# Kernel optimization log

Hardware: AMD Instinct MI355X
Metric: run time of the kernel (lower is better)

Reference implementation:

```python
import jax, jax.numpy as jnp
import numpy as np

CUTOFF = 5.0
P = 6               # envelope polynomial power
NUM_RBF = 6
NUM_SBF = 7
EMBED = 128
TYPE_EMBED = 64
OUT_EMBED = 256
INT_EMBED = 64      # angle_int_embed_size
BASIS_EMBED = 8
N_BLOCKS = 4
N_DENSE_OUT = 3
N_RES_BEFORE = 1
N_RES_AFTER = 2
N_SPECIES = 16
NUM_TARGETS = 1
N_ATOMS = 4096
N_EDGES = 65536
N_TRIPLETS = 524288

# first 6 positive roots of spherical Bessel j_l, l = 0..6
BESSEL_ZEROS = np.array([
    [3.141593, 6.283185, 9.424778, 12.566371, 15.707963, 18.849556],
    [4.493409, 7.725252, 10.904122, 14.066194, 17.220755, 20.371303],
    [5.763459, 9.095011, 12.322941, 15.514603, 18.689036, 21.853874],
    [6.987932, 10.417119, 13.698023, 16.923621, 20.121806, 23.304247],
    [8.182561, 11.704907, 15.039665, 18.301256, 21.525418, 24.727566],
    [9.355812, 12.966530, 16.354710, 19.653152, 22.904551, 26.126750],
    [10.512835, 14.207392, 17.647975, 20.983463, 24.262768, 27.507868]], dtype=np.float32)

act = jax.nn.silu  # swish


def envelope(x):
    a = -(P + 1) * (P + 2) / 2.0
    b = float(P * (P + 2))
    c = -P * (P + 1) / 2.0
    env = 1.0 / x + a * x ** (P - 1) + b * x ** P + c * x ** (P + 1)
    return jnp.where(x < 1.0, env, 0.0)


def radial_bessel(d):
    # d: (E,) -> (E, NUM_RBF)
    x = d / CUTOFF
    n = jnp.arange(1, NUM_RBF + 1, dtype=jnp.float32)
    return np.float32(np.sqrt(2.0 / CUTOFF)) * envelope(x)[:, None] * jnp.sin(jnp.pi * n[None, :] * x[:, None])


def spherical_basis(d_kj, angles, triplet_mask):
    # d_kj: (T,), angles: (T,) -> (T, NUM_SBF * NUM_RBF)
    x = jnp.maximum(d_kj / CUTOFF, 1e-6)
    env = envelope(x)
    zeros = jnp.asarray(BESSEL_ZEROS)
    radial = []
    for l in range(NUM_SBF):
        a = zeros[l][None, :] * x[:, None]           # (T, NUM_RBF)
        j0 = jnp.sin(a) / a
        if l == 0:
            radial.append(j0)
            continue
        j1 = jnp.sin(a) / a ** 2 - jnp.cos(a) / a
        jm2, jm1 = j0, j1
        for ll in range(2, l + 1):
            jm2, jm1 = jm1, (2 * ll - 1) / a * jm1 - jm2
        radial.append(jm1)
    radial = jnp.stack(radial, axis=1)               # (T, NUM_SBF, NUM_RBF)
    ct = jnp.cos(angles)
    Pl = [jnp.ones_like(ct), ct]
    for l in range(2, NUM_SBF):
        Pl.append(((2 * l - 1) * ct * Pl[l - 1] - (l - 1) * Pl[l - 2]) / l)
    sph = jnp.stack([np.float32(np.sqrt((2 * l + 1) / (4.0 * np.pi))) * Pl[l] for l in range(NUM_SBF)], axis=1)  # (T, NUM_SBF)
    sbf = (env[:, None, None] * radial * sph[:, :, None]).reshape(-1, NUM_SBF * NUM_RBF)
    return jnp.where(triplet_mask[:, None], sbf, 0.0)


def _forward(distances, angles, species_embed, emb_rbf_w, emb_rbf_b, emb_dense_w, emb_dense_b,
             out_rbf_w, out_up_w, out_dense_w, out_dense_b, out_final_w,
             int_ji_w, int_ji_b, int_kj_w, int_kj_b, int_rbf1_w, int_rbf2_w, int_down_w,
             int_sbf1_w, int_sbf2_w, int_up_w, int_res1_w, int_res1_b, int_skip_w, int_skip_b,
             int_res2_w, int_res2_b,
             species, idx_i, idx_j, reduce_to_ji, expand_to_kj, edge_mask, triplet_mask):
    n_particles = species.shape[0]
    n_edges = distances.shape[0]
    d = jnp.where(edge_mask, distances, 2.0 * CUTOFF)       # masked edges -> env = 0
    rbf = radial_bessel(d)                                  # (E, 6)
    sbf = spherical_basis(d[expand_to_kj], angles, triplet_mask)  # (T, 42)

    # embedding block
    h = species_embed[species]                              # (N, 64)
    rbf_emb = rbf @ emb_rbf_w + emb_rbf_b                   # (E, 128)
    m = act(jnp.concatenate([h[idx_j], h[idx_i], rbf_emb], axis=-1) @ emb_dense_w + emb_dense_b)

    def output_block(i, msg):
        atom = jax.ops.segment_sum((rbf @ out_rbf_w[i]) * msg, idx_i, num_segments=n_particles)
        atom = atom @ out_up_w[i]
        for k in range(N_DENSE_OUT):
            atom = act(atom @ out_dense_w[i, k] + out_dense_b[i, k])
        return atom @ out_final_w[i]

    out = output_block(0, m)
    for i in range(N_BLOCKS):
        x_ji = act(m @ int_ji_w[i] + int_ji_b[i])
        x_kj = act(m @ int_kj_w[i] + int_kj_b[i])
        x_kj = x_kj * ((rbf @ int_rbf1_w[i]) @ int_rbf2_w[i])
        x_kj = act(x_kj @ int_down_w[i])                    # (E, 64)
        x_kj = x_kj[expand_to_kj] * ((sbf @ int_sbf1_w[i]) @ int_sbf2_w[i])  # (T, 64)
        x_kj = jax.ops.segment_sum(x_kj, reduce_to_ji, num_segments=n_edges)
        x_kj = act(x_kj @ int_up_w[i])
        hm = x_ji + x_kj
        for r in range(N_RES_BEFORE):
            hm = hm + act(act(hm @ int_res1_w[i, r, 0] + int_res1_b[i, r, 0]) @ int_res1_w[i, r, 1] + int_res1_b[i, r, 1])
        m = act(hm @ int_skip_w[i] + int_skip_b[i]) + m
        for r in range(N_RES_AFTER):
            m = m + act(act(m @ int_res2_w[i, r, 0] + int_res2_b[i, r, 0]) @ int_res2_w[i, r, 1] + int_res2_b[i, r, 1])
        out = out + output_block(i + 1, m)
    return out


def setup_inputs() -> dict:
    key = jax.random.key(0)
    ks = iter(jax.random.split(key, 40))
    def nrm(shape, fan_in):
        return jax.random.normal(next(ks), shape, dtype=jnp.float32) / np.float32(np.sqrt(fan_in))
    inp = {}
    inp['distances'] = 0.5 + 4.45 * jax.random.uniform(next(ks), (N_EDGES,), dtype=jnp.float32)
    inp['angles'] = jnp.pi * jax.random.uniform(next(ks), (N_TRIPLETS,), dtype=jnp.float32)
    inp['species_embed'] = jax.random.normal(next(ks), (N_SPECIES, TYPE_EMBED), dtype=jnp.float32)
    inp['emb_rbf_w'] = nrm((NUM_RBF, EMBED), NUM_RBF)
    inp['emb_rbf_b'] = jnp.zeros((EMBED,), jnp.float32)
    inp['emb_dense_w'] = nrm((2 * TYPE_EMBED + EMBED, EMBED), 2 * TYPE_EMBED + EMBED)
    inp['emb_dense_b'] = jnp.zeros((EMBED,), jnp.float32)
    nb1 = N_BLOCKS + 1
    inp['out_rbf_w'] = nrm((nb1, NUM_RBF, EMBED), NUM_RBF)
    inp['out_up_w'] = nrm((nb1, EMBED, OUT_EMBED), EMBED)
    inp['out_dense_w'] = nrm((nb1, N_DENSE_OUT, OUT_EMBED, OUT_EMBED), OUT_EMBED)
    inp['out_dense_b'] = jnp.zeros((nb1, N_DENSE_OUT, OUT_EMBED), jnp.float32)
    inp['out_final_w'] = nrm((nb1, OUT_EMBED, NUM_TARGETS), OUT_EMBED)
    inp['int_ji_w'] = nrm((N_BLOCKS, EMBED, EMBED), EMBED)
    inp['int_ji_b'] = jnp.zeros((N_BLOCKS, EMBED), jnp.float32)
    inp['int_kj_w'] = nrm((N_BLOCKS, EMBED, EMBED), EMBED)
    inp['int_kj_b'] = jnp.zeros((N_BLOCKS, EMBED), jnp.float32)
    inp['int_rbf1_w'] = nrm((N_BLOCKS, NUM_RBF, BASIS_EMBED), NUM_RBF)
    inp['int_rbf2_w'] = nrm((N_BLOCKS, BASIS_EMBED, EMBED), BASIS_EMBED)
    inp['int_down_w'] = nrm((N_BLOCKS, EMBED, INT_EMBED), EMBED)
    inp['int_sbf1_w'] = nrm((N_BLOCKS, NUM_SBF * NUM_RBF, BASIS_EMBED), NUM_SBF * NUM_RBF)
    inp['int_sbf2_w'] = nrm((N_BLOCKS, BASIS_EMBED, INT_EMBED), BASIS_EMBED)
    inp['int_up_w'] = nrm((N_BLOCKS, INT_EMBED, EMBED), INT_EMBED)
    inp['int_res1_w'] = nrm((N_BLOCKS, N_RES_BEFORE, 2, EMBED, EMBED), EMBED)
    inp['int_res1_b'] = jnp.zeros((N_BLOCKS, N_RES_BEFORE, 2, EMBED), jnp.float32)
    inp['int_skip_w'] = nrm((N_BLOCKS, EMBED, EMBED), EMBED)
    inp['int_skip_b'] = jnp.zeros((N_BLOCKS, EMBED), jnp.float32)
    inp['int_res2_w'] = nrm((N_BLOCKS, N_RES_AFTER, 2, EMBED, EMBED), EMBED)
    inp['int_res2_b'] = jnp.zeros((N_BLOCKS, N_RES_AFTER, 2, EMBED), jnp.float32)
    inp['species'] = jax.random.randint(next(ks), (N_ATOMS,), 0, N_SPECIES)
    inp['idx_i'] = jax.random.randint(next(ks), (N_EDGES,), 0, N_ATOMS)
    inp['idx_j'] = jax.random.randint(next(ks), (N_EDGES,), 0, N_ATOMS)
    inp['reduce_to_ji'] = jax.random.randint(next(ks), (N_TRIPLETS,), 0, N_EDGES)
    inp['expand_to_kj'] = jax.random.randint(next(ks), (N_TRIPLETS,), 0, N_EDGES)
    inp['edge_mask'] = jnp.ones((N_EDGES,), dtype=bool)
    inp['triplet_mask'] = jnp.ones((N_TRIPLETS,), dtype=bool)
    return inp


def reference(distances, angles, species_embed, emb_rbf_w, emb_rbf_b, emb_dense_w, emb_dense_b,
              out_rbf_w, out_up_w, out_dense_w, out_dense_b, out_final_w,
              int_ji_w, int_ji_b, int_kj_w, int_kj_b, int_rbf1_w, int_rbf2_w, int_down_w,
              int_sbf1_w, int_sbf2_w, int_up_w, int_res1_w, int_res1_b, int_skip_w, int_skip_b,
              int_res2_w, int_res2_b,
              species, idx_i, idx_j, reduce_to_ji, expand_to_kj, edge_mask, triplet_mask):
    return _forward(distances, angles, species_embed, emb_rbf_w, emb_rbf_b, emb_dense_w, emb_dense_b,
                    out_rbf_w, out_up_w, out_dense_w, out_dense_b, out_final_w,
                    int_ji_w, int_ji_b, int_kj_w, int_kj_b, int_rbf1_w, int_rbf2_w, int_down_w,
                    int_sbf1_w, int_sbf2_w, int_up_w, int_res1_w, int_res1_b, int_skip_w, int_skip_b,
                    int_res2_w, int_res2_b,
                    species, idx_i, idx_j, reduce_to_ji, expand_to_kj, edge_mask, triplet_mask)
```

## Files before the change

kernel.cpp:

```cpp
#include <hip/hip_runtime.h>
#include <cmath>

typedef __attribute__((ext_vector_type(8))) short bfrag;
typedef __attribute__((ext_vector_type(4))) float f32x4;

__device__ __forceinline__ float silu_f(float x) {
    return x / (1.0f + __expf(-x));
}
__device__ __forceinline__ unsigned short f2bf(float f) {
    unsigned u = __float_as_uint(f);
    unsigned r = (u + 0x7fff + ((u >> 16) & 1)) >> 16;
    return (unsigned short)r;
}
__device__ __forceinline__ float bf2f(unsigned short h) {
    return __uint_as_float(((unsigned)h) << 16);
}
__device__ __forceinline__ unsigned packbf2(float lo, float hi) {
    return ((unsigned)f2bf(hi) << 16) | (unsigned)f2bf(lo);
}

__device__ __forceinline__ void put_split4(unsigned short* Ah, unsigned short* Al,
                                           int row, int col, float4 v) {
    short4 h4, l4;
    unsigned short h;
    h = f2bf(v.x); h4.x = (short)h; l4.x = (short)f2bf(v.x - bf2f(h));
    h = f2bf(v.y); h4.y = (short)h; l4.y = (short)f2bf(v.y - bf2f(h));
    h = f2bf(v.z); h4.z = (short)h; l4.z = (short)f2bf(v.z - bf2f(h));
    h = f2bf(v.w); h4.w = (short)h; l4.w = (short)f2bf(v.w - bf2f(h));
    *(short4*)&Ah[row * 136 + col] = h4;
    *(short4*)&Al[row * 136 + col] = l4;
}

template <int KSTEPS, int S, int NS>
__device__ __forceinline__ void mfma_stage(
    const unsigned short* Ah, const unsigned short* Al,
    const unsigned short* __restrict__ Whi, const unsigned short* __restrict__ Wlo,
    int Kdim, int arow0, int bcol0, int r16, int kg, f32x4 (&acc)[S][NS]) {
    #pragma unroll
    for (int s = 0; s < S; s++)
        #pragma unroll
        for (int ns = 0; ns < NS; ns++) acc[s][ns] = (f32x4)0.f;
    #pragma unroll
    for (int ks = 0; ks < KSTEPS; ks++) {
        int k0 = ks * 32;
        bfrag bh[NS], bl[NS];
        #pragma unroll
        for (int ns = 0; ns < NS; ns++) {
            size_t bo = (size_t)(bcol0 + ns * 16 + r16) * Kdim + k0 + kg * 8;
            bh[ns] = *(const bfrag*)&Whi[bo];
            bl[ns] = *(const bfrag*)&Wlo[bo];
        }
        #pragma unroll
        for (int s = 0; s < S; s++) {
            int ao = (arow0 + s * 16 + r16) * 136 + k0 + kg * 8;
            bfrag ah = *(const bfrag*)&Ah[ao];
            bfrag al = *(const bfrag*)&Al[ao];
            #pragma unroll
            for (int ns = 0; ns < NS; ns++) {
                acc[s][ns] = __builtin_amdgcn_mfma_f32_16x16x32_bf16(ah, bh[ns], acc[s][ns], 0, 0, 0);
                acc[s][ns] = __builtin_amdgcn_mfma_f32_16x16x32_bf16(ah, bl[ns], acc[s][ns], 0, 0, 0);
                acc[s][ns] = __builtin_amdgcn_mfma_f32_16x16x32_bf16(al, bh[ns], acc[s][ns], 0, 0, 0);
            }
        }
    }
}

__device__ __forceinline__ void frag_store_lds(unsigned short* Ah, unsigned short* Al,
                                               const f32x4 (&v)[4][2], int arow0, int bcol0,
                                               int r16, int kg) {
    #pragma unroll
    for (int s = 0; s < 4; s++)
        #pragma unroll
        for (int ns = 0; ns < 2; ns++)
            #pragma unroll
            for (int r = 0; r < 4; r++) {
                int row = arow0 + s * 16 + kg * 4 + r;
                int col = bcol0 + ns * 16 + r16;
                float f = v[s][ns][r];
                unsigned short h = f2bf(f);
                Ah[row * 136 + col] = h;
                Al[row * 136 + col] = f2bf(f - bf2f(h));
            }
}

__device__ __forceinline__ void frag_store_lds_act(unsigned short* Ah, unsigned short* Al,
                                                   const f32x4 (&a)[4][2], float bb0, float bb1,
                                                   int arow0, int bcol0, int r16, int kg) {
    float b[2] = {bb0, bb1};
    #pragma unroll
    for (int s = 0; s < 4; s++)
        #pragma unroll
        for (int ns = 0; ns < 2; ns++)
            #pragma unroll
            for (int r = 0; r < 4; r++) {
                int row = arow0 + s * 16 + kg * 4 + r;
                int col = bcol0 + ns * 16 + r16;
                float f = silu_f(a[s][ns][r] + b[ns]);
                unsigned short h = f2bf(f);
                Ah[row * 136 + col] = h;
                Al[row * 136 + col] = f2bf(f - bf2f(h));
            }
}

__global__ __launch_bounds__(256) void rbf_kernel(const float* __restrict__ d,
                                                  float* __restrict__ rbf, int E) {
    int e = blockIdx.x * 256 + threadIdx.x;
    if (e >= E) return;
    float x = d[e] * 0.2f;
    float env = 0.0f;
    if (x < 1.0f) {
        float x2 = x * x;
        float x5 = x2 * x2 * x;
        env = 1.0f / x + x5 * (-28.0f + x * (48.0f - 21.0f * x));
    }
    const float SQ = 0.63245553f;
    float px = 3.14159265358979f * x;
    #pragma unroll
    for (int n = 1; n <= 6; n++) {
        rbf[e * 6 + n - 1] = SQ * env * sinf(px * (float)n);
    }
}

__global__ __launch_bounds__(128) void embed_pre_kernel(
    const float* __restrict__ se, const float* __restrict__ erw,
// ... 46 lines not shown
    const float* Wb = W + (size_t)b * K * N;
    int tid = threadIdx.x;
    int r = tid >> 3, cg = tid & 7;
    float4 v = *(const float4*)&Wb[(size_t)(k0 + r) * N + n0 + cg * 4];
    t[r][cg * 4 + 0] = v.x;
    t[r][cg * 4 + 1] = v.y;
    t[r][cg * 4 + 2] = v.z;
    t[r][cg * 4 + 3] = v.w;
    __syncthreads();
    int nl = tid >> 3, kg = tid & 7;
    short4 h4, l4;
    float f0 = t[kg * 4 + 0][nl], f1 = t[kg * 4 + 1][nl];
    float f2 = t[kg * 4 + 2][nl], f3 = t[kg * 4 + 3][nl];
    unsigned short h;
    h = f2bf(f0); h4.x = (short)h; l4.x = (short)f2bf(f0 - bf2f(h));
    h = f2bf(f1); h4.y = (short)h; l4.y = (short)f2bf(f1 - bf2f(h));
    h = f2bf(f2); h4.z = (short)h; l4.z = (short)f2bf(f2 - bf2f(h));
    h = f2bf(f3); h4.w = (short)h; l4.w = (short)f2bf(f3 - bf2f(h));
    size_t o = ((size_t)b * N + n0 + nl) * K + k0 + kg * 4;
    *(short4*)&hi[o] = h4;
    *(short4*)&lo[o] = l4;
}

template <int BN, int ACT, int BIAS, int RES>
__global__ __launch_bounds__(BN * 4) void mfma_gemm(
    const float* __restrict__ X, const unsigned short* __restrict__ Whi,
    const unsigned short* __restrict__ Wlo,
    const float* __restrict__ bias, const float* __restrict__ resid,
    float* __restrict__ Y, int M, int K, int N) {
    constexpr int T = BN * 4;
    constexpr int WC = BN / 32;
    constexpr int AP = 1024 / T;
    __shared__ unsigned short Ah[128 * 40];
    __shared__ unsigned short Al[128 * 40];
    __shared__ unsigned short Bh[BN * 40];
    __shared__ unsigned short Bl[BN * 40];

    int tid = threadIdx.x;
    int bm = blockIdx.x * 128, bn = blockIdx.y * BN;
    int wid = tid >> 6, lane = tid & 63;
    int wr = wid / WC, wc = wid % WC;
    int r16 = lane & 15, kg = lane >> 4;

    f32x4 acc[4][2];
    #pragma unroll
    for (int s = 0; s < 4; s++)
        #pragma unroll
        for (int ns = 0; ns < 2; ns++) acc[s][ns] = (f32x4)0.f;

    int brow = tid >> 2, bkg = tid & 3;

    for (int k0 = 0; k0 < K; k0 += 32) {
        float4 av[AP];
        #pragma unroll
        for (int p = 0; p < AP; p++) {
            int idx = tid + p * T;
            int row = idx >> 3, cg = idx & 7;
            av[p] = *(const float4*)&X[(size_t)(bm + row) * K + k0 + cg * 4];
        }
        float4 bh = *(const float4*)&Whi[(size_t)(bn + brow) * K + k0 + bkg * 8];
        float4 bl = *(const float4*)&Wlo[(size_t)(bn + brow) * K + k0 + bkg * 8];
        __syncthreads();
        #pragma unroll
        for (int p = 0; p < AP; p++) {
            int idx = tid + p * T;
            int row = idx >> 3, cg = idx & 7;
            float fv[4] = {av[p].x, av[p].y, av[p].z, av[p].w};
            short4 h4, l4;
            unsigned short h;
            h = f2bf(fv[0]); h4.x = (short)h; l4.x = (short)f2bf(fv[0] - bf2f(h));
            h = f2bf(fv[1]); h4.y = (short)h; l4.y = (short)f2bf(fv[1] - bf2f(h));
            h = f2bf(fv[2]); h4.z = (short)h; l4.z = (short)f2bf(fv[2] - bf2f(h));
            h = f2bf(fv[3]); h4.w = (short)h; l4.w = (short)f2bf(fv[3] - bf2f(h));
            *(short4*)&Ah[row * 40 + cg * 4] = h4;
            *(short4*)&Al[row * 40 + cg * 4] = l4;
        }
        *(float4*)&Bh[brow * 40 + bkg * 8] = bh;
        *(float4*)&Bl[brow * 40 + bkg * 8] = bl;
        __syncthreads();

        bfrag bhf[2], blf[2];
        #pragma unroll
        for (int ns = 0; ns < 2; ns++) {
            int br = wc * 32 + ns * 16 + r16;
            bhf[ns] = *(const bfrag*)&Bh[br * 40 + kg * 8];
            blf[ns] = *(const bfrag*)&Bl[br * 40 + kg * 8];
        }
        #pragma unroll
        for (int s = 0; s < 4; s++) {
            int ar = wr * 64 + s * 16 + r16;
            bfrag ah = *(const bfrag*)&Ah[ar * 40 + kg * 8];
            bfrag al = *(const bfrag*)&Al[ar * 40 + kg * 8];
            #pragma unroll
            for (int ns = 0; ns < 2; ns++) {
                acc[s][ns] = __builtin_amdgcn_mfma_f32_16x16x32_bf16(ah, bhf[ns], acc[s][ns], 0, 0, 0);
                acc[s][ns] = __builtin_amdgcn_mfma_f32_16x16x32_bf16(ah, blf[ns], acc[s][ns], 0, 0, 0);
                acc[s][ns] = __builtin_amdgcn_mfma_f32_16x16x32_bf16(al, bhf[ns], acc[s][ns], 0, 0, 0);
            }
        }
    }

    #pragma unroll
    for (int s = 0; s < 4; s++) {
        int row0 = bm + wr * 64 + s * 16 + kg * 4;
        #pragma unroll
        for (int ns = 0; ns < 2; ns++) {
            int col = bn + wc * 32 + ns * 16 + r16;
            float bv = 0.f;
            if (BIAS) bv = bias[col];
            #pragma unroll
            for (int r = 0; r < 4; r++) {
                size_t o = (size_t)(row0 + r) * N + col;
                float v = acc[s][ns][r] + bv;
                if (ACT) v = silu_f(v);
                if (RES) v += resid[o];
                Y[o] = v;
            }
        }
    }
}

__global__ __launch_bounds__(512, 2) void downpath_kernel(
    const float* __restrict__ m, const float* __restrict__ rbf,
    const float* __restrict__ rbf1, const float* __restrict__ rbf2,
    const unsigned short* __restrict__ jih, const unsigned short* __restrict__ jil,
    const float* __restrict__ jib,
    const unsigned short* __restrict__ kjh, const unsigned short* __restrict__ kjl,
    const float* __restrict__ kjb,
    const unsigned short* __restrict__ dnh, const unsigned short* __restrict__ dnl,
    float* __restrict__ xji, float* __restrict__ xdown) {
    __shared__ unsigned short Ah[128 * 136];
    __shared__ unsigned short Al[128 * 136];
    __shared__ float G8s[128][8];
    int tid = threadIdx.x, bm = blockIdx.x * 128;
    int wid = tid >> 6, lane = tid & 63;
    int wr = wid >> 2, wc = wid & 3;
    int r16 = lane & 15, kg = lane >> 4;
    int arow0 = wr * 64, bcol0 = wc * 32;

    #pragma unroll
    for (int p = 0; p < 8; p++) {
        int idx = tid + p * 512, row = idx >> 5, cg = idx & 31;
        float4 v = *(const float4*)&m[(size_t)(bm + row) * 128 + cg * 4];
        put_split4(Ah, Al, row, cg * 4, v);
    }
    if (tid < 128) {
        float rv[6];
        #pragma unroll
        for (int k = 0; k < 6; k++) rv[k] = rbf[(size_t)(bm + tid) * 6 + k];
        #pragma unroll
        for (int p = 0; p < 8; p++) {
            float a = 0.f;
            #pragma unroll
            for (int k = 0; k < 6; k++) a += rv[k] * rbf1[k * 8 + p];
            G8s[tid][p] = a;
        }
    }
    __syncthreads();

    f32x4 acc[4][2];
    mfma_stage<4, 4, 2>(Ah, Al, jih, jil, 128, arow0, bcol0, r16, kg, acc);
    {
        float b[2] = {jib[bcol0 + r16], jib[bcol0 + 16 + r16]};
        #pragma unroll
        for (int s = 0; s < 4; s++)
            #pragma unroll
            for (int ns = 0; ns < 2; ns++)
                #pragma unroll
                for (int r = 0; r < 4; r++) {
                    int row = arow0 + s * 16 + kg * 4 + r;
                    int col = bcol0 + ns * 16 + r16;
                    xji[(size_t)(bm + row) * 128 + col] = silu_f(acc[s][ns][r] + b[ns]);
                }
    }
    mfma_stage<4, 4, 2>(Ah, Al, kjh, kjl, 128, arow0, bcol0, r16, kg, acc);
    {
        float w2[2][8];
        #pragma unroll
        for (int ns = 0; ns < 2; ns++)
            #pragma unroll
            for (int p = 0; p < 8; p++) w2[ns][p] = rbf2[p * 128 + bcol0 + ns * 16 + r16];
        float b[2] = {kjb[bcol0 + r16], kjb[bcol0 + 16 + r16]};
        #pragma unroll
        for (int s = 0; s < 4; s++)
            #pragma unroll
            for (int ns = 0; ns < 2; ns++)
                #pragma unroll
                for (int r = 0; r < 4; r++) {
                    int row = arow0 + s * 16 + kg * 4 + r;
                    float g = 0.f;
                    #pragma unroll
                    for (int p = 0; p < 8; p++) g = fmaf(G8s[row][p], w2[ns][p], g);
                    acc[s][ns][r] = silu_f(acc[s][ns][r] + b[ns]) * g;
                }
    }
    __syncthreads();
    frag_store_lds(Ah, Al, acc, arow0, bcol0, r16, kg);
    __syncthreads();
    {
        int wr2 = wid >> 1, wc2 = wid & 1;
        int ar2 = wr2 * 32, bc2 = wc2 * 32;
        f32x4 a2[2][2];
        mfma_stage<4, 2, 2>(Ah, Al, dnh, dnl, 128, ar2, bc2, r16, kg, a2);
        #pragma unroll
        for (int s = 0; s < 2; s++)
            #pragma unroll
            for (int ns = 0; ns < 2; ns++)
                #pragma unroll
                for (int r = 0; r < 4; r++) {
                    int row = ar2 + s * 16 + kg * 4 + r;
                    int col = bc2 + ns * 16 + r16;
                    xdown[(size_t)(bm + row) * 64 + col] = silu_f(a2[s][ns][r]);
                }
    }
}

__global__ __launch_bounds__(512, 2) void chain_kernel(
    const float* __restrict__ seg, const float* __restrict__ xji, float* __restrict__ m,
    const unsigned short* __restrict__ uph, const unsigned short* __restrict__ upl,
    const unsigned short* __restrict__ r1h, const unsigned short* __restrict__ r1l,
    const float* __restrict__ r1b,
    const unsigned short* __restrict__ skh, const unsigned short* __restrict__ skl,
    const float* __restrict__ skb,
    const unsigned short* __restrict__ r2h, const unsigned short* __restrict__ r2l,
    const float* __restrict__ r2b) {
    __shared__ unsigned short Ah[128 * 136];
    __shared__ unsigned short Al[128 * 136];
    int tid = threadIdx.x, bm = blockIdx.x * 128;
    int wid = tid >> 6, lane = tid & 63;
    int wr = wid >> 2, wc = wid & 3;
    int r16 = lane & 15, kg = lane >> 4;
    int arow0 = wr * 64, bcol0 = wc * 32;

    #pragma unroll
    for (int p = 0; p < 4; p++) {
        int idx = tid + p * 512, row = idx >> 4, cg = idx & 15;
        float4 v = *(const float4*)&seg[(size_t)(bm + row) * 64 + cg * 4];
        put_split4(Ah, Al, row, cg * 4, v);
    }
    __syncthreads();

    f32x4 acc[4][2], res[4][2];

    mfma_stage<2, 4, 2>(Ah, Al, uph, upl, 64, arow0, bcol0, r16, kg, acc);
    #pragma unroll
    for (int s = 0; s < 4; s++)
        #pragma unroll
        for (int ns = 0; ns < 2; ns++)
            #pragma unroll
            for (int r = 0; r < 4; r++) {
                int row = arow0 + s * 16 + kg * 4 + r;
                int col = bcol0 + ns * 16 + r16;
                res[s][ns][r] = silu_f(acc[s][ns][r]) + xji[(size_t)(bm + row) * 128 + col];
            }
    __syncthreads();
    frag_store_lds(Ah, Al, res, arow0, bcol0, r16, kg);
    __syncthreads();

    mfma_stage<4, 4, 2>(Ah, Al, r1h, r1l, 128, arow0, bcol0, r16, kg, acc);
    __syncthreads();
    frag_store_lds_act(Ah, Al, acc, r1b[bcol0 + r16], r1b[bcol0 + 16 + r16],
                       arow0, bcol0, r16, kg);
    __syncthreads();
    mfma_stage<4, 4, 2>(Ah, Al, r1h + 16384, r1l + 16384, 128, arow0, bcol0, r16, kg, acc);
    {
        float b[2] = {r1b[128 + bcol0 + r16], r1b[128 + bcol0 + 16 + r16]};
        #pragma unroll
        for (int s = 0; s < 4; s++)
            #pragma unroll
            for (int ns = 0; ns < 2; ns++)
                #pragma unroll
                for (int r = 0; r < 4; r++)
                    res[s][ns][r] += silu_f(acc[s][ns][r] + b[ns]);
    }
    __syncthreads();
    frag_store_lds(Ah, Al, res, arow0, bcol0, r16, kg);
    __syncthreads();

    mfma_stage<4, 4, 2>(Ah, Al, skh, skl, 128, arow0, bcol0, r16, kg, acc);
    {
        float b[2] = {skb[bcol0 + r16], skb[bcol0 + 16 + r16]};
        #pragma unroll
        for (int s = 0; s < 4; s++)
            #pragma unroll
            for (int ns = 0; ns < 2; ns++)
                #pragma unroll
                for (int r = 0; r < 4; r++) {
                    int row = arow0 + s * 16 + kg * 4 + r;
                    int col = bcol0 + ns * 16 + r16;
                    res[s][ns][r] = silu_f(acc[s][ns][r] + b[ns]) + m[(size_t)(bm + row) * 128 + col];
                }
    }
    __syncthreads();
    frag_store_lds(Ah, Al, res, arow0, bcol0, r16, kg);
    __syncthreads();

    #pragma unroll
    for (int rr = 0; rr < 2; rr++) {
        const unsigned short* wh = r2h + (size_t)rr * 2 * 16384;
        const unsigned short* wl = r2l + (size_t)rr * 2 * 16384;
        const float* bb = r2b + (size_t)rr * 2 * 128;
        mfma_stage<4, 4, 2>(Ah, Al, wh, wl, 128, arow0, bcol0, r16, kg, acc);
        __syncthreads();
        frag_store_lds_act(Ah, Al, acc, bb[bcol0 + r16], bb[bcol0 + 16 + r16],
                           arow0, bcol0, r16, kg);
        __syncthreads();
        mfma_stage<4, 4, 2>(Ah, Al, wh + 16384, wl + 16384, 128, arow0, bcol0, r16, kg, acc);
        {
            float b[2] = {bb[128 + bcol0 + r16], bb[128 + bcol0 + 16 + r16]};
            #pragma unroll
            for (int s = 0; s < 4; s++)
                #pragma unroll
                for (int ns = 0; ns < 2; ns++)
                    #pragma unroll
                    for (int r = 0; r < 4; r++)
                        res[s][ns][r] += silu_f(acc[s][ns][r] + b[ns]);
        }
        if (rr == 0) {
            __syncthreads();
            frag_store_lds(Ah, Al, res, arow0, bcol0, r16, kg);
            __syncthreads();
        }
    }
    #pragma unroll
    for (int s = 0; s < 4; s++)
        #pragma unroll
        for (int ns = 0; ns < 2; ns++)
            #pragma unroll
            for (int r = 0; r < 4; r++) {
                int row = arow0 + s * 16 + kg * 4 + r;
                int col = bcol0 + ns * 16 + r16;
                m[(size_t)(bm + row) * 128 + col] = res[s][ns][r];
            }
}

__global__ __launch_bounds__(256) void outseg_kernel(
    const float* __restrict__ rbf, const float* __restrict__ orw,
    const float* __restrict__ m, const int* __restrict__ idx_i,
    float* __restrict__ atom) {
    int gid = blockIdx.x * 256 + threadIdx.x;
    int e = gid >> 7, c = gid & 127;
    float s = 0.f;
    #pragma unroll
    for (int k = 0; k < 6; k++) s += rbf[e * 6 + k] * orw[k * 128 + c];
    atomicAdd(&atom[(size_t)idx_i[e] * 128 + c], s * m[gid]);
}

__global__ __launch_bounds__(64) void final_kernel(
    const float* __restrict__ atom, const float* __restrict__ wf,
    float* __restrict__ out) {
    int a = blockIdx.x, l = threadIdx.x;
    float s = 0.f;
    #pragma unroll
    for (int q = 0; q < 4; q++) s += atom[(size_t)a * 256 + q * 64 + l] * wf[q * 64 + l];
    #pragma unroll
    for (int off = 32; off; off >>= 1) s += __shfl_down(s, off, 64);
// ... 276 lines not shown
    sbf_pre_kernel<<<T / 256, 256, 0, stream>>>(distances, angles, perm, ekjs,
                                                int_sbf1_w, t32, T);

    wconv_kernel<<<dim3(4, 4, 4), 256, 0, stream>>>(int_ji_w, ji_h, ji_l, 128, 128);
    wconv_kernel<<<dim3(4, 4, 4), 256, 0, stream>>>(int_kj_w, kj_h, kj_l, 128, 128);
    wconv_kernel<<<dim3(2, 4, 4), 256, 0, stream>>>(int_down_w, dn_h, dn_l, 128, 64);
    wconv_kernel<<<dim3(4, 2, 4), 256, 0, stream>>>(int_up_w, up_h, up_l, 64, 128);
    wconv_kernel<<<dim3(4, 4, 8), 256, 0, stream>>>(int_res1_w, r1_h, r1_l, 128, 128);
    wconv_kernel<<<dim3(4, 4, 4), 256, 0, stream>>>(int_skip_w, sk_h, sk_l, 128, 128);
    wconv_kernel<<<dim3(4, 4, 16), 256, 0, stream>>>(int_res2_w, r2_h, r2_l, 128, 128);
    wconv_kernel<<<dim3(8, 4, 5), 256, 0, stream>>>(out_up_w, ou_h, ou_l, 128, 256);
    wconv_kernel<<<dim3(8, 8, 15), 256, 0, stream>>>(out_dense_w, od_h, od_l, 256, 256);

    rbf_kernel<<<E / 256, 256, 0, stream>>>(distances, rbf, E);
    embed_pre_kernel<<<1, 128, 0, stream>>>(species_emb, emb_rbf_w, emb_rbf_b,
                                            emb_dense_w, HWj, HWi, W3, b3);
    embed_kernel<<<E * 128 / 256, 256, 0, stream>>>(rbf, species, idx_i, idx_j,
                                                    HWj, HWi, W3, b3, emb_dense_b, m);

    auto outblock = [&](int i, const float* msg) {
        hipMemsetAsync(atom1, 0, (size_t)NA * 128 * sizeof(float), stream);
        outseg_kernel<<<E * 128 / 256, 256, 0, stream>>>(
            rbf, out_rbf_w + (size_t)i * 6 * 128, msg, idx_i, atom1);
        mfma_gemm<128, 0, 0, 0><<<dim3(NA / 128, 2), 512, 0, stream>>>(
            atom1, ou_h + (size_t)i * 32768, ou_l + (size_t)i * 32768,
            nullptr, nullptr, atom2, NA, 128, 256);
        mfma_gemm<128, 1, 1, 0><<<dim3(NA / 128, 2), 512, 0, stream>>>(
            atom2, od_h + ((size_t)i * 3 + 0) * 65536, od_l + ((size_t)i * 3 + 0) * 65536,
            out_dense_b + ((size_t)i * 3 + 0) * 256, nullptr, atom3, NA, 256, 256);
        mfma_gemm<128, 1, 1, 0><<<dim3(NA / 128, 2), 512, 0, stream>>>(
            atom3, od_h + ((size_t)i * 3 + 1) * 65536, od_l + ((size_t)i * 3 + 1) * 65536,
            out_dense_b + ((size_t)i * 3 + 1) * 256, nullptr, atom2, NA, 256, 256);
        mfma_gemm<128, 1, 1, 0><<<dim3(NA / 128, 2), 512, 0, stream>>>(
            atom2, od_h + ((size_t)i * 3 + 2) * 65536, od_l + ((size_t)i * 3 + 2) * 65536,
            out_dense_b + ((size_t)i * 3 + 2) * 256, nullptr, atom3, NA, 256, 256);
        final_kernel<<<NA, 64, 0, stream>>>(atom3, out_final_w + (size_t)i * 256, out);
    };

    outblock(0, m);

    for (int i = 0; i < 4; i++) {
        downpath_kernel<<<E / 128, 512, 0, stream>>>(
            m, rbf, int_rbf1_w + (size_t)i * 48, int_rbf2_w + (size_t)i * 1024,
            ji_h + (size_t)i * 16384, ji_l + (size_t)i * 16384, int_ji_b + (size_t)i * 128,
            kj_h + (size_t)i * 16384, kj_l + (size_t)i * 16384, int_kj_b + (size_t)i * 128,
            dn_h + (size_t)i * 8192, dn_l + (size_t)i * 8192,
            A, D);
        seg_gather_kernel<<<E * 64 / 256, 256, 0, stream>>>(
            t32 + (size_t)i * T * 8, ekjs, rows, D,
            int_sbf2_w + (size_t)i * 8 * 64, seg, E);
        chain_kernel<<<E / 128, 512, 0, stream>>>(
            seg, A, m,
            up_h + (size_t)i * 8192, up_l + (size_t)i * 8192,
            r1_h + (size_t)i * 32768, r1_l + (size_t)i * 32768, int_res1_b + (size_t)i * 256,
            sk_h + (size_t)i * 16384, sk_l + (size_t)i * 16384, int_skip_b + (size_t)i * 128,
            r2_h + (size_t)i * 65536, r2_l + (size_t)i * 65536, int_res2_b + (size_t)i * 512);
// ... 4 lines not shown
```

Measured before the change: 1.634 ms.

## Drop activation low-bf16 split, swap MFMA operands for row-contiguous vector stores

Activations are now converted to a single bf16 value instead of a hi/lo pair. Each GEMM therefore issues two MFMAs per tile instead of three, and the LDS footprint for activations is halved. MFMA operands are swapped (weights as A, activations as B) so each lane owns four consecutive output columns, which allows float4 bias loads, residual loads and output stores. Weight fragments in the standalone GEMM are read straight from global memory rather than staged through LDS. This costs accuracy, since activations lose their low-order correction bits.

```diff
diff --git a/kernel.cpp b/kernel.cpp
--- a/kernel.cpp
+++ b/kernel.cpp
@@ -18,22 +18,16 @@
 __device__ __forceinline__ unsigned packbf2(float lo, float hi) {
     return ((unsigned)f2bf(hi) << 16) | (unsigned)f2bf(lo);
 }
-
-__device__ __forceinline__ void put_split4(unsigned short* Ah, unsigned short* Al,
-                                           int row, int col, float4 v) {
-    short4 h4, l4;
-    unsigned short h;
-    h = f2bf(v.x); h4.x = (short)h; l4.x = (short)f2bf(v.x - bf2f(h));
-    h = f2bf(v.y); h4.y = (short)h; l4.y = (short)f2bf(v.y - bf2f(h));
-    h = f2bf(v.z); h4.z = (short)h; l4.z = (short)f2bf(v.z - bf2f(h));
-    h = f2bf(v.w); h4.w = (short)h; l4.w = (short)f2bf(v.w - bf2f(h));
-    *(short4*)&Ah[row * 136 + col] = h4;
-    *(short4*)&Al[row * 136 + col] = l4;
-}
-
-template <int KSTEPS, int S, int NS>
-__device__ __forceinline__ void mfma_stage(
-    const unsigned short* Ah, const unsigned short* Al,
+__device__ __forceinline__ short4 hi4f(float a, float b, float c, float d) {
+    short4 h;
+    h.x = (short)f2bf(a); h.y = (short)f2bf(b);
+    h.z = (short)f2bf(c); h.w = (short)f2bf(d);
+    return h;
+}
+
+template <int KSTEPS, int S, int NS, int ST>
+__device__ __forceinline__ void mfma_stage_T(
+    const unsigned short* Xs,
     const unsigned short* __restrict__ Whi, const unsigned short* __restrict__ Wlo,
     int Kdim, int arow0, int bcol0, int r16, int kg, f32x4 (&acc)[S][NS]) {
     #pragma unroll
@@ -43,63 +37,23 @@
     #pragma unroll
     for (int ks = 0; ks < KSTEPS; ks++) {
         int k0 = ks * 32;
-        bfrag bh[NS], bl[NS];
+        bfrag wh[NS], wl[NS];
         #pragma unroll
         for (int ns = 0; ns < NS; ns++) {
-            size_t bo = (size_t)(bcol0 + ns * 16 + r16) * Kdim + k0 + kg * 8;
-            bh[ns] = *(const bfrag*)&Whi[bo];
-            bl[ns] = *(const bfrag*)&Wlo[bo];
+            size_t o = (size_t)(bcol0 + ns * 16 + r16) * Kdim + k0 + kg * 8;
+            wh[ns] = *(const bfrag*)&Whi[o];
+            wl[ns] = *(const bfrag*)&Wlo[o];
         }
         #pragma unroll
         for (int s = 0; s < S; s++) {
-            int ao = (arow0 + s * 16 + r16) * 136 + k0 + kg * 8;
-            bfrag ah = *(const bfrag*)&Ah[ao];
-            bfrag al = *(const bfrag*)&Al[ao];
+            bfrag xh = *(const bfrag*)&Xs[(arow0 + s * 16 + r16) * ST + k0 + kg * 8];
             #pragma unroll
             for (int ns = 0; ns < NS; ns++) {
-                acc[s][ns] = __builtin_amdgcn_mfma_f32_16x16x32_bf16(ah, bh[ns], acc[s][ns], 0, 0, 0);
-                acc[s][ns] = __builtin_amdgcn_mfma_f32_16x16x32_bf16(ah, bl[ns], acc[s][ns], 0, 0, 0);
-                acc[s][ns] = __builtin_amdgcn_mfma_f32_16x16x32_bf16(al, bh[ns], acc[s][ns], 0, 0, 0);
-            }
-        }
-    }
-}
-
-__device__ __forceinline__ void frag_store_lds(unsigned short* Ah, unsigned short* Al,
-                                               const f32x4 (&v)[4][2], int arow0, int bcol0,
-                                               int r16, int kg) {
-    #pragma unroll
-    for (int s = 0; s < 4; s++)
-        #pragma unroll
-        for (int ns = 0; ns < 2; ns++)
-            #pragma unroll
-            for (int r = 0; r < 4; r++) {
-                int row = arow0 + s * 16 + kg * 4 + r;
-                int col = bcol0 + ns * 16 + r16;
-                float f = v[s][ns][r];
-                unsigned short h = f2bf(f);
-                Ah[row * 136 + col] = h;
-                Al[row * 136 + col] = f2bf(f - bf2f(h));
-            }
-}
-
-__device__ __forceinline__ void frag_store_lds_act(unsigned short* Ah, unsigned short* Al,
-                                                   const f32x4 (&a)[4][2], float bb0, float bb1,
-                                                   int arow0, int bcol0, int r16, int kg) {
-    float b[2] = {bb0, bb1};
-    #pragma unroll
-    for (int s = 0; s < 4; s++)
-        #pragma unroll
-        for (int ns = 0; ns < 2; ns++)
-            #pragma unroll
-            for (int r = 0; r < 4; r++) {
-                int row = arow0 + s * 16 + kg * 4 + r;
-                int col = bcol0 + ns * 16 + r16;
-                float f = silu_f(a[s][ns][r] + b[ns]);
-                unsigned short h = f2bf(f);
-                Ah[row * 136 + col] = h;
-                Al[row * 136 + col] = f2bf(f - bf2f(h));
-            }
+                acc[s][ns] = __builtin_amdgcn_mfma_f32_16x16x32_bf16(wh[ns], xh, acc[s][ns], 0, 0, 0);
+                acc[s][ns] = __builtin_amdgcn_mfma_f32_16x16x32_bf16(wl[ns], xh, acc[s][ns], 0, 0, 0);
+            }
+        }
+    }
 }
 
 __global__ __launch_bounds__(256) void rbf_kernel(const float* __restrict__ d,
@@ -192,25 +146,19 @@
     *(short4*)&lo[o] = l4;
 }
 
-template <int BN, int ACT, int BIAS, int RES>
-__global__ __launch_bounds__(BN * 4) void mfma_gemm(
+template <int ACT, int BIAS, int RES>
+__global__ __launch_bounds__(512, 2) void mfma_gemmT(
     const float* __restrict__ X, const unsigned short* __restrict__ Whi,
     const unsigned short* __restrict__ Wlo,
     const float* __restrict__ bias, const float* __restrict__ resid,
     float* __restrict__ Y, int M, int K, int N) {
-    constexpr int T = BN * 4;
-    constexpr int WC = BN / 32;
-    constexpr int AP = 1024 / T;
-    __shared__ unsigned short Ah[128 * 40];
-    __shared__ unsigned short Al[128 * 40];
-    __shared__ unsigned short Bh[BN * 40];
-    __shared__ unsigned short Bl[BN * 40];
-
+    __shared__ unsigned short Xs[128 * 40];
     int tid = threadIdx.x;
-    int bm = blockIdx.x * 128, bn = blockIdx.y * BN;
+    int bm = blockIdx.x * 128, bn = blockIdx.y * 128;
     int wid = tid >> 6, lane = tid & 63;
-    int wr = wid / WC, wc = wid % WC;
+    int wr = wid >> 2, wc = wid & 3;
     int r16 = lane & 15, kg = lane >> 4;
+    int arow0 = wr * 64, bcol0 = wc * 32;
 
     f32x4 acc[4][2];
     #pragma unroll
@@ -218,74 +166,57 @@
         #pragma unroll
         for (int ns = 0; ns < 2; ns++) acc[s][ns] = (f32x4)0.f;
 
-    int brow = tid >> 2, bkg = tid & 3;
-
     for (int k0 = 0; k0 < K; k0 += 32) {
-        float4 av[AP];
-        #pragma unroll
-        for (int p = 0; p < AP; p++) {
-            int idx = tid + p * T;
+        #pragma unroll
+        for (int p = 0; p < 2; p++) {
+            int idx = tid + p * 512;
             int row = idx >> 3, cg = idx & 7;
-            av[p] = *(const float4*)&X[(size_t)(bm + row) * K + k0 + cg * 4];
-        }
-        float4 bh = *(const float4*)&Whi[(size_t)(bn + brow) * K + k0 + bkg * 8];
-        float4 bl = *(const float4*)&Wlo[(size_t)(bn + brow) * K + k0 + bkg * 8];
+            float4 v = *(const float4*)&X[(size_t)(bm + row) * K + k0 + cg * 4];
+            *(short4*)&Xs[row * 40 + cg * 4] = hi4f(v.x, v.y, v.z, v.w);
+        }
         __syncthreads();
-        #pragma unroll
-        for (int p = 0; p < AP; p++) {
-            int idx = tid + p * T;
-            int row = idx >> 3, cg = idx & 7;
-            float fv[4] = {av[p].x, av[p].y, av[p].z, av[p].w};
-            short4 h4, l4;
-            unsigned short h;
-            h = f2bf(fv[0]); h4.x = (short)h; l4.x = (short)f2bf(fv[0] - bf2f(h));
-            h = f2bf(fv[1]); h4.y = (short)h; l4.y = (short)f2bf(fv[1] - bf2f(h));
-            h = f2bf(fv[2]); h4.z = (short)h; l4.z = (short)f2bf(fv[2] - bf2f(h));
-            h = f2bf(fv[3]); h4.w = (short)h; l4.w = (short)f2bf(fv[3] - bf2f(h));
-            *(short4*)&Ah[row * 40 + cg * 4] = h4;
-            *(short4*)&Al[row * 40 + cg * 4] = l4;
-        }
-        *(float4*)&Bh[brow * 40 + bkg * 8] = bh;
-        *(float4*)&Bl[brow * 40 + bkg * 8] = bl;
+        bfrag wh[2], wl[2];
+        #pragma unroll
+        for (int ns = 0; ns < 2; ns++) {
+            size_t o = (size_t)(bn + bcol0 + ns * 16 + r16) * K + k0 + kg * 8;
+            wh[ns] = *(const bfrag*)&Whi[o];
+            wl[ns] = *(const bfrag*)&Wlo[o];
+        }
+        #pragma unroll
+        for (int s = 0; s < 4; s++) {
+            bfrag xh = *(const bfrag*)&Xs[(arow0 + s * 16 + r16) * 40 + kg * 8];
+            #pragma unroll
+            for (int ns = 0; ns < 2; ns++) {
+                acc[s][ns] = __builtin_amdgcn_mfma_f32_16x16x32_bf16(wh[ns], xh, acc[s][ns], 0, 0, 0);
+                acc[s][ns] = __builtin_amdgcn_mfma_f32_16x16x32_bf16(wl[ns], xh, acc[s][ns], 0, 0, 0);
+            }
+        }
         __syncthreads();
-
-        bfrag bhf[2], blf[2];
+    }
+    #pragma unroll
+    for (int s = 0; s < 4; s++) {
+        int mm = bm + arow0 + s * 16 + r16;
         #pragma unroll
         for (int ns = 0; ns < 2; ns++) {
-            int br = wc * 32 + ns * 16 + r16;
-            bhf[ns] = *(const bfrag*)&Bh[br * 40 + kg * 8];
-            blf[ns] = *(const bfrag*)&Bl[br * 40 + kg * 8];
-        }
-        #pragma unroll
-        for (int s = 0; s < 4; s++) {
-            int ar = wr * 64 + s * 16 + r16;
-            bfrag ah = *(const bfrag*)&Ah[ar * 40 + kg * 8];
-            bfrag al = *(const bfrag*)&Al[ar * 40 + kg * 8];
-            #pragma unroll
-            for (int ns = 0; ns < 2; ns++) {
-                acc[s][ns] = __builtin_amdgcn_mfma_f32_16x16x32_bf16(ah, bhf[ns], acc[s][ns], 0, 0, 0);
-                acc[s][ns] = __builtin_amdgcn_mfma_f32_16x16x32_bf16(ah, blf[ns], acc[s][ns], 0, 0, 0);
-                acc[s][ns] = __builtin_amdgcn_mfma_f32_16x16x32_bf16(al, bhf[ns], acc[s][ns], 0, 0, 0);
-            }
-        }
-    }
-
-    #pragma unroll
-    for (int s = 0; s < 4; s++) {
-        int row0 = bm + wr * 64 + s * 16 + kg * 4;
-        #pragma unroll
-        for (int ns = 0; ns < 2; ns++) {
-            int col = bn + wc * 32 + ns * 16 + r16;
-            float bv = 0.f;
-            if (BIAS) bv = bias[col];
+            int n0 = bn + bcol0 + ns * 16 + kg * 4;
+            float bv[4] = {0.f, 0.f, 0.f, 0.f};
+            if (BIAS) {
+                float4 b4 = *(const float4*)&bias[n0];
+                bv[0] = b4.x; bv[1] = b4.y; bv[2] = b4.z; bv[3] = b4.w;
+            }
+            float4 o;
+            float* op = (float*)&o;
             #pragma unroll
             for (int r = 0; r < 4; r++) {
-                size_t o = (size_t)(row0 + r) * N + col;
-                float v = acc[s][ns][r] + bv;
+                float v = acc[s][ns][r] + bv[r];
                 if (ACT) v = silu_f(v);
-                if (RES) v += resid[o];
-                Y[o] = v;
-            }
+                op[r] = v;
+            }
+            if (RES) {
+                float4 rv = *(const float4*)&resid[(size_t)mm * N + n0];
+                o.x += rv.x; o.y += rv.y; o.z += rv.z; o.w += rv.w;
+            }
+            *(float4*)&Y[(size_t)mm * N + n0] = o;
         }
     }
 }
@@ -299,9 +230,9 @@
     const float* __restrict__ kjb,
     const unsigned short* __restrict__ dnh, const unsigned short* __restrict__ dnl,
     float* __restrict__ xji, float* __restrict__ xdown) {
-    __shared__ unsigned short Ah[128 * 136];
-    __shared__ unsigned short Al[128 * 136];
-    __shared__ float G8s[128][8];
+    __shared__ unsigned short Xs[128 * 136];
+    __shared__ float G8t[8][128];
+    __shared__ float Rs[8][128];
     int tid = threadIdx.x, bm = blockIdx.x * 128;
     int wid = tid >> 6, lane = tid & 63;
     int wr = wid >> 2, wc = wid & 3;
@@ -312,7 +243,7 @@
     for (int p = 0; p < 8; p++) {
         int idx = tid + p * 512, row = idx >> 5, cg = idx & 31;
         float4 v = *(const float4*)&m[(size_t)(bm + row) * 128 + cg * 4];
-        put_split4(Ah, Al, row, cg * 4, v);
+        *(short4*)&Xs[row * 136 + cg * 4] = hi4f(v.x, v.y, v.z, v.w);
     }
     if (tid < 128) {
         float rv[6];
@@ -323,65 +254,77 @@
             float a = 0.f;
             #pragma unroll
             for (int k = 0; k < 6; k++) a += rv[k] * rbf1[k * 8 + p];
-            G8s[tid][p] = a;
-        }
-    }
+            G8t[p][tid] = a;
+        }
+    }
+    for (int i = tid; i < 1024; i += 512) Rs[i >> 7][i & 127] = rbf2[i];
     __syncthreads();
 
     f32x4 acc[4][2];
-    mfma_stage<4, 4, 2>(Ah, Al, jih, jil, 128, arow0, bcol0, r16, kg, acc);
-    {
-        float b[2] = {jib[bcol0 + r16], jib[bcol0 + 16 + r16]};
-        #pragma unroll
-        for (int s = 0; s < 4; s++)
-            #pragma unroll
-            for (int ns = 0; ns < 2; ns++)
+    mfma_stage_T<4, 4, 2, 136>(Xs, jih, jil, 128, arow0, bcol0, r16, kg, acc);
+    #pragma unroll
+    for (int s = 0; s < 4; s++) {
+        int mm = bm + arow0 + s * 16 + r16;
+        #pragma unroll
+        for (int ns = 0; ns < 2; ns++) {
+            int n0 = bcol0 + ns * 16 + kg * 4;
+            float4 b4 = *(const float4*)&jib[n0];
+            float4 o;
+            o.x = silu_f(acc[s][ns][0] + b4.x);
+            o.y = silu_f(acc[s][ns][1] + b4.y);
+            o.z = silu_f(acc[s][ns][2] + b4.z);
+            o.w = silu_f(acc[s][ns][3] + b4.w);
+            *(float4*)&xji[(size_t)mm * 128 + n0] = o;
+        }
+    }
+    mfma_stage_T<4, 4, 2, 136>(Xs, kjh, kjl, 128, arow0, bcol0, r16, kg, acc);
+    f32x4 val[4][2];
+    #pragma unroll
+    for (int s = 0; s < 4; s++) {
+        int mrow = arow0 + s * 16 + r16;
+        float g8v[8];
+        #pragma unroll
+        for (int p = 0; p < 8; p++) g8v[p] = G8t[p][mrow];
+        #pragma unroll
+        for (int ns = 0; ns < 2; ns++) {
+            int n0 = bcol0 + ns * 16 + kg * 4;
+            float4 b4 = *(const float4*)&kjb[n0];
+            float bb[4] = {b4.x, b4.y, b4.z, b4.w};
+            #pragma unroll
+            for (int r = 0; r < 4; r++) {
+                float g = 0.f;
                 #pragma unroll
-                for (int r = 0; r < 4; r++) {
-                    int row = arow0 + s * 16 + kg * 4 + r;
-                    int col = bcol0 + ns * 16 + r16;
-                    xji[(size_t)(bm + row) * 128 + col] = silu_f(acc[s][ns][r] + b[ns]);
-                }
-    }
-    mfma_stage<4, 4, 2>(Ah, Al, kjh, kjl, 128, arow0, bcol0, r16, kg, acc);
-    {
-        float w2[2][8];
+                for (int p = 0; p < 8; p++) g = fmaf(g8v[p], Rs[p][n0 + r], g);
+                val[s][ns][r] = silu_f(acc[s][ns][r] + bb[r]) * g;
+            }
+        }
+    }
+    __syncthreads();
+    #pragma unroll
+    for (int s = 0; s < 4; s++)
         #pragma unroll
         for (int ns = 0; ns < 2; ns++)
-            #pragma unroll
-            for (int p = 0; p < 8; p++) w2[ns][p] = rbf2[p * 128 + bcol0 + ns * 16 + r16];
-        float b[2] = {kjb[bcol0 + r16], kjb[bcol0 + 16 + r16]};
-        #pragma unroll
-        for (int s = 0; s < 4; s++)
-            #pragma unroll
-            for (int ns = 0; ns < 2; ns++)
-                #pragma unroll
-                for (int r = 0; r < 4; r++) {
-                    int row = arow0 + s * 16 + kg * 4 + r;
-                    float g = 0.f;
-                    #pragma unroll
-                    for (int p = 0; p < 8; p++) g = fmaf(G8s[row][p], w2[ns][p], g);
-                    acc[s][ns][r] = silu_f(acc[s][ns][r] + b[ns]) * g;
-                }
-    }
-    __syncthreads();
-    frag_store_lds(Ah, Al, acc, arow0, bcol0, r16, kg);
+            *(short4*)&Xs[(arow0 + s * 16 + r16) * 136 + bcol0 + ns * 16 + kg * 4] =
+                hi4f(val[s][ns][0], val[s][ns][1], val[s][ns][2], val[s][ns][3]);
     __syncthreads();
     {
         int wr2 = wid >> 1, wc2 = wid & 1;
-        int ar2 = wr2 * 32, bc2 = wc2 * 32;
         f32x4 a2[2][2];
-        mfma_stage<4, 2, 2>(Ah, Al, dnh, dnl, 128, ar2, bc2, r16, kg, a2);
-        #pragma unroll
-        for (int s = 0; s < 2; s++)
-            #pragma unroll
-            for (int ns = 0; ns < 2; ns++)
-                #pragma unroll
-                for (int r = 0; r < 4; r++) {
-                    int row = ar2 + s * 16 + kg * 4 + r;
-                    int col = bc2 + ns * 16 + r16;
-                    xdown[(size_t)(bm + row) * 64 + col] = silu_f(a2[s][ns][r]);
-                }
+        mfma_stage_T<4, 2, 2, 136>(Xs, dnh, dnl, 128, wr2 * 32, wc2 * 32, r16, kg, a2);
+        #pragma unroll
+        for (int s = 0; s < 2; s++) {
+            int mm = bm + wr2 * 32 + s * 16 + r16;
+            #pragma unroll
+            for (int ns = 0; ns < 2; ns++) {
+                int n0 = wc2 * 32 + ns * 16 + kg * 4;
+                float4 o;
+                o.x = silu_f(a2[s][ns][0]);
+                o.y = silu_f(a2[s][ns][1]);
+                o.z = silu_f(a2[s][ns][2]);
+                o.w = silu_f(a2[s][ns][3]);
+                *(float4*)&xdown[(size_t)mm * 64 + n0] = o;
+            }
+        }
     }
 }
 
@@ -394,8 +337,7 @@
     const float* __restrict__ skb,
     const unsigned short* __restrict__ r2h, const unsigned short* __restrict__ r2l,
     const float* __restrict__ r2b) {
-    __shared__ unsigned short Ah[128 * 136];
-    __shared__ unsigned short Al[128 * 136];
+    __shared__ unsigned short Xs[128 * 136];
     int tid = threadIdx.x, bm = blockIdx.x * 128;
     int wid = tid >> 6, lane = tid & 63;
     int wr = wid >> 2, wc = wid & 3;
@@ -406,63 +348,91 @@
     for (int p = 0; p < 4; p++) {
         int idx = tid + p * 512, row = idx >> 4, cg = idx & 15;
         float4 v = *(const float4*)&seg[(size_t)(bm + row) * 64 + cg * 4];
-        put_split4(Ah, Al, row, cg * 4, v);
+        *(short4*)&Xs[row * 136 + cg * 4] = hi4f(v.x, v.y, v.z, v.w);
     }
     __syncthreads();
 
     f32x4 acc[4][2], res[4][2];
 
-    mfma_stage<2, 4, 2>(Ah, Al, uph, upl, 64, arow0, bcol0, r16, kg, acc);
+    mfma_stage_T<2, 4, 2, 136>(Xs, uph, upl, 64, arow0, bcol0, r16, kg, acc);
+    #pragma unroll
+    for (int s = 0; s < 4; s++) {
+        int mm = bm + arow0 + s * 16 + r16;
+        #pragma unroll
+        for (int ns = 0; ns < 2; ns++) {
+            int n0 = bcol0 + ns * 16 + kg * 4;
+            float4 xv = *(const float4*)&xji[(size_t)mm * 128 + n0];
+            res[s][ns][0] = silu_f(acc[s][ns][0]) + xv.x;
+            res[s][ns][1] = silu_f(acc[s][ns][1]) + xv.y;
+            res[s][ns][2] = silu_f(acc[s][ns][2]) + xv.z;
+            res[s][ns][3] = silu_f(acc[s][ns][3]) + xv.w;
+        }
+    }
+    __syncthreads();
     #pragma unroll
     for (int s = 0; s < 4; s++)
         #pragma unroll
         for (int ns = 0; ns < 2; ns++)
-            #pragma unroll
-            for (int r = 0; r < 4; r++) {
-                int row = arow0 + s * 16 + kg * 4 + r;
-                int col = bcol0 + ns * 16 + r16;
-                res[s][ns][r] = silu_f(acc[s][ns][r]) + xji[(size_t)(bm + row) * 128 + col];
-            }
-    __syncthreads();
-    frag_store_lds(Ah, Al, res, arow0, bcol0, r16, kg);
-    __syncthreads();
-
-    mfma_stage<4, 4, 2>(Ah, Al, r1h, r1l, 128, arow0, bcol0, r16, kg, acc);
-    __syncthreads();
-    frag_store_lds_act(Ah, Al, acc, r1b[bcol0 + r16], r1b[bcol0 + 16 + r16],
-                       arow0, bcol0, r16, kg);
-    __syncthreads();
-    mfma_stage<4, 4, 2>(Ah, Al, r1h + 16384, r1l + 16384, 128, arow0, bcol0, r16, kg, acc);
-    {
-        float b[2] = {r1b[128 + bcol0 + r16], r1b[128 + bcol0 + 16 + r16]};
-        #pragma unroll
-        for (int s = 0; s < 4; s++)
-            #pragma unroll
-            for (int ns = 0; ns < 2; ns++)
-                #pragma unroll
-                for (int r = 0; r < 4; r++)
-                    res[s][ns][r] += silu_f(acc[s][ns][r] + b[ns]);
-    }
-    __syncthreads();
-    frag_store_lds(Ah, Al, res, arow0, bcol0, r16, kg);
-    __syncthreads();
-
-    mfma_stage<4, 4, 2>(Ah, Al, skh, skl, 128, arow0, bcol0, r16, kg, acc);
-    {
-        float b[2] = {skb[bcol0 + r16], skb[bcol0 + 16 + r16]};
-        #pragma unroll
-        for (int s = 0; s < 4; s++)
-            #pragma unroll
-            for (int ns = 0; ns < 2; ns++)
-                #pragma unroll
-                for (int r = 0; r < 4; r++) {
-                    int row = arow0 + s * 16 + kg * 4 + r;
-                    int col = bcol0 + ns * 16 + r16;
-                    res[s][ns][r] = silu_f(acc[s][ns][r] + b[ns]) + m[(size_t)(bm + row) * 128 + col];
-                }
-    }
-    __syncthreads();
-    frag_store_lds(Ah, Al, res, arow0, bcol0, r16, kg);
+            *(short4*)&Xs[(arow0 + s * 16 + r16) * 136 + bcol0 + ns * 16 + kg * 4] =
+                hi4f(res[s][ns][0], res[s][ns][1], res[s][ns][2], res[s][ns][3]);
+    __syncthreads();
+
+    mfma_stage_T<4, 4, 2, 136>(Xs, r1h, r1l, 128, arow0, bcol0, r16, kg, acc);
+    __syncthreads();
+    #pragma unroll
+    for (int s = 0; s < 4; s++)
+        #pragma unroll
+        for (int ns = 0; ns < 2; ns++) {
+            int n0 = bcol0 + ns * 16 + kg * 4;
+            float4 b4 = *(const float4*)&r1b[n0];
+            *(short4*)&Xs[(arow0 + s * 16 + r16) * 136 + n0] =
+                hi4f(silu_f(acc[s][ns][0] + b4.x), silu_f(acc[s][ns][1] + b4.y),
+                     silu_f(acc[s][ns][2] + b4.z), silu_f(acc[s][ns][3] + b4.w));
+        }
+    __syncthreads();
+    mfma_stage_T<4, 4, 2, 136>(Xs, r1h + 16384, r1l + 16384, 128, arow0, bcol0, r16, kg, acc);
+    #pragma unroll
+    for (int s = 0; s < 4; s++)
+        #pragma unroll
+        for (int ns = 0; ns < 2; ns++) {
+            int n0 = bcol0 + ns * 16 + kg * 4;
+            float4 b4 = *(const float4*)&r1b[128 + n0];
+            res[s][ns][0] += silu_f(acc[s][ns][0] + b4.x);
+            res[s][ns][1] += silu_f(acc[s][ns][1] + b4.y);
+            res[s][ns][2] += silu_f(acc[s][ns][2] + b4.z);
+            res[s][ns][3] += silu_f(acc[s][ns][3] + b4.w);
+        }
+    __syncthreads();
+    #pragma unroll
+    for (int s = 0; s < 4; s++)
+        #pragma unroll
+        for (int ns = 0; ns < 2; ns++)
+            *(short4*)&Xs[(arow0 + s * 16 + r16) * 136 + bcol0 + ns * 16 + kg * 4] =
+                hi4f(res[s][ns][0], res[s][ns][1], res[s][ns][2], res[s][ns][3]);
+    __syncthreads();
+
+    mfma_stage_T<4, 4, 2, 136>(Xs, skh, skl, 128, arow0, bcol0, r16, kg, acc);
+    #pragma unroll
+    for (int s = 0; s < 4; s++) {
+        int mm = bm + arow0 + s * 16 + r16;
+        #pragma unroll
+        for (int ns = 0; ns < 2; ns++) {
+            int n0 = bcol0 + ns * 16 + kg * 4;
+            float4 b4 = *(const float4*)&skb[n0];
+            float4 mv = *(const float4*)&m[(size_t)mm * 128 + n0];
+            res[s][ns][0] = silu_f(acc[s][ns][0] + b4.x) + mv.x;
+            res[s][ns][1] = silu_f(acc[s][ns][1] + b4.y) + mv.y;
+            res[s][ns][2] = silu_f(acc[s][ns][2] + b4.z) + mv.z;
+            res[s][ns][3] = silu_f(acc[s][ns][3] + b4.w) + mv.w;
+        }
+    }
+    __syncthreads();
+    #pragma unroll
+    for (int s = 0; s < 4; s++)
+        #pragma unroll
+        for (int ns = 0; ns < 2; ns++)
+            *(short4*)&Xs[(arow0 + s * 16 + r16) * 136 + bcol0 + ns * 16 + kg * 4] =
+                hi4f(res[s][ns][0], res[s][ns][1], res[s][ns][2], res[s][ns][3]);
     __syncthreads();
 
     #pragma unroll
@@ -470,38 +440,54 @@
         const unsigned short* wh = r2h + (size_t)rr * 2 * 16384;
         const unsigned short* wl = r2l + (size_t)rr * 2 * 16384;
         const float* bb = r2b + (size_t)rr * 2 * 128;
-        mfma_stage<4, 4, 2>(Ah, Al, wh, wl, 128, arow0, bcol0, r16, kg, acc);
+        mfma_stage_T<4, 4, 2, 136>(Xs, wh, wl, 128, arow0, bcol0, r16, kg, acc);
         __syncthreads();
-        frag_store_lds_act(Ah, Al, acc, bb[bcol0 + r16], bb[bcol0 + 16 + r16],
-                           arow0, bcol0, r16, kg);
+        #pragma unroll
+        for (int s = 0; s < 4; s++)
+            #pragma unroll
+            for (int ns = 0; ns < 2; ns++) {
+                int n0 = bcol0 + ns * 16 + kg * 4;
+                float4 b4 = *(const float4*)&bb[n0];
+                *(short4*)&Xs[(arow0 + s * 16 + r16) * 136 + n0] =
+                    hi4f(silu_f(acc[s][ns][0] + b4.x), silu_f(acc[s][ns][1] + b4.y),
+                         silu_f(acc[s][ns][2] + b4.z), silu_f(acc[s][ns][3] + b4.w));
+            }
         __syncthreads();
-        mfma_stage<4, 4, 2>(Ah, Al, wh + 16384, wl + 16384, 128, arow0, bcol0, r16, kg, acc);
-        {
-            float b[2] = {bb[128 + bcol0 + r16], bb[128 + bcol0 + 16 + r16]};
+        mfma_stage_T<4, 4, 2, 136>(Xs, wh + 16384, wl + 16384, 128, arow0, bcol0, r16, kg, acc);
+        #pragma unroll
+        for (int s = 0; s < 4; s++)
+            #pragma unroll
+            for (int ns = 0; ns < 2; ns++) {
+                int n0 = bcol0 + ns * 16 + kg * 4;
+                float4 b4 = *(const float4*)&bb[128 + n0];
+                res[s][ns][0] += silu_f(acc[s][ns][0] + b4.x);
+                res[s][ns][1] += silu_f(acc[s][ns][1] + b4.y);
+                res[s][ns][2] += silu_f(acc[s][ns][2] + b4.z);
+                res[s][ns][3] += silu_f(acc[s][ns][3] + b4.w);
+            }
+        if (rr == 0) {
+            __syncthreads();
             #pragma unroll
             for (int s = 0; s < 4; s++)
                 #pragma unroll
                 for (int ns = 0; ns < 2; ns++)
-                    #pragma unroll
-                    for (int r = 0; r < 4; r++)
-                        res[s][ns][r] += silu_f(acc[s][ns][r] + b[ns]);
-        }
-        if (rr == 0) {
+                    *(short4*)&Xs[(arow0 + s * 16 + r16) * 136 + bcol0 + ns * 16 + kg * 4] =
+                        hi4f(res[s][ns][0], res[s][ns][1], res[s][ns][2], res[s][ns][3]);
             __syncthreads();
-            frag_store_lds(Ah, Al, res, arow0, bcol0, r16, kg);
-            __syncthreads();
-        }
-    }
-    #pragma unroll
-    for (int s = 0; s < 4; s++)
-        #pragma unroll
-        for (int ns = 0; ns < 2; ns++)
-            #pragma unroll
-            for (int r = 0; r < 4; r++) {
-                int row = arow0 + s * 16 + kg * 4 + r;
-                int col = bcol0 + ns * 16 + r16;
-                m[(size_t)(bm + row) * 128 + col] = res[s][ns][r];
-            }
+        }
+    }
+    #pragma unroll
+    for (int s = 0; s < 4; s++) {
+        int mm = bm + arow0 + s * 16 + r16;
+        #pragma unroll
+        for (int ns = 0; ns < 2; ns++) {
+            int n0 = bcol0 + ns * 16 + kg * 4;
+            float4 o;
+            o.x = res[s][ns][0]; o.y = res[s][ns][1];
+            o.z = res[s][ns][2]; o.w = res[s][ns][3];
+            *(float4*)&m[(size_t)mm * 128 + n0] = o;
+        }
+    }
 }
 
 __global__ __launch_bounds__(256) void outseg_kernel(
@@ -824,16 +810,16 @@
         hipMemsetAsync(atom1, 0, (size_t)NA * 128 * sizeof(float), stream);
         outseg_kernel<<<E * 128 / 256, 256, 0, stream>>>(
             rbf, out_rbf_w + (size_t)i * 6 * 128, msg, idx_i, atom1);
-        mfma_gemm<128, 0, 0, 0><<<dim3(NA / 128, 2), 512, 0, stream>>>(
+        mfma_gemmT<0, 0, 0><<<dim3(NA / 128, 2), 512, 0, stream>>>(
             atom1, ou_h + (size_t)i * 32768, ou_l + (size_t)i * 32768,
             nullptr, nullptr, atom2, NA, 128, 256);
-        mfma_gemm<128, 1, 1, 0><<<dim3(NA / 128, 2), 512, 0, stream>>>(
+        mfma_gemmT<1, 1, 0><<<dim3(NA / 128, 2), 512, 0, stream>>>(
             atom2, od_h + ((size_t)i * 3 + 0) * 65536, od_l + ((size_t)i * 3 + 0) * 65536,
             out_dense_b + ((size_t)i * 3 + 0) * 256, nullptr, atom3, NA, 256, 256);
-        mfma_gemm<128, 1, 1, 0><<<dim3(NA / 128, 2), 512, 0, stream>>>(
+        mfma_gemmT<1, 1, 0><<<dim3(NA / 128, 2), 512, 0, stream>>>(
             atom3, od_h + ((size_t)i * 3 + 1) * 65536, od_l + ((size_t)i * 3 + 1) * 65536,
             out_dense_b + ((size_t)i * 3 + 1) * 256, nullptr, atom2, NA, 256, 256);
-        mfma_gemm<128, 1, 1, 0><<<dim3(NA / 128, 2), 512, 0, stream>>>(
+        mfma_gemmT<1, 1, 0><<<dim3(NA / 128, 2), 512, 0, stream>>>(
             atom2, od_h + ((size_t)i * 3 + 2) * 65536, od_l + ((size_t)i * 3 + 2) * 65536,
             out_dense_b + ((size_t)i * 3 + 2) * 256, nullptr, atom3, NA, 256, 256);
         final_kernel<<<NA, 64, 0, stream>>>(atom3, out_final_w + (size_t)i * 256, out);
```

New measurement: 1.646 ms. About the same (+0.7%).
